# Kernel optimization log

Hardware: AMD Instinct MI355X
Metric: run time of the kernel (lower is better)

Reference implementation:

```python
import jax, jax.numpy as jnp
import numpy as np

N_HEADS = 32
HEAD_DIM = 128
TOPK = 2048
FP8_MAX = 448.0  # e4m3 max, per-token-head q quantization scale
NEG = -1e30


def _hadamard_matrix(d):
    # Sylvester construction; matches fast-hadamard-transform ordering.
    h = np.array([[1.0]], dtype=np.float32)
    while h.shape[0] < d:
        h = np.block([[h, h], [h, -h]])
    return jnp.asarray(h * d ** -0.5)  # rotate_activation scale = d^-0.5


def setup_inputs() -> dict:
    key = jax.random.key(0)
    k0, k1, k2, k3 = jax.random.split(key, 4)
    T, HID = 4096, 2048
    hidden_states = jax.random.normal(k0, (T, HID), jnp.float32)
    wq = jax.random.normal(k1, (HID, N_HEADS * HEAD_DIM), jnp.float32) * 0.02
    wk = jax.random.normal(k2, (HID, HEAD_DIM), jnp.float32) * 0.02
    ww = jax.random.normal(k3, (HID, N_HEADS), jnp.float32) * 0.02
    # Ragged causal KV bounds (compute_cu_seqlen_kv_bounds_with_cache, no cache):
    seq_lens = np.array([1024, 3072], dtype=np.int64)
    offs = np.concatenate([[0], np.cumsum(seq_lens)])
    batch_ids = np.repeat(np.arange(len(seq_lens)), seq_lens)
    ks = offs[batch_ids]                                   # start of own sequence
    local = np.arange(T) - np.repeat(offs[:-1], seq_lens)  # local query position
    ke = ks + local + 1                                    # causal end (exclusive)
    return {
        'hidden_states': hidden_states, 'wq': wq, 'wk': wk, 'ww': ww,
        'cu_seqlen_ks': jnp.asarray(ks, jnp.int32),
        'cu_seqlen_ke': jnp.asarray(ke, jnp.int32),
    }


def reference(hidden_states, wq, wk, ww, cu_seqlen_ks, cu_seqlen_ke):
    T = hidden_states.shape[0]
    Hm = _hadamard_matrix(HEAD_DIM)
    # Projections + Hadamard rotation (rotate_activation)
    q = (hidden_states @ wq).reshape(T, N_HEADS, HEAD_DIM) @ Hm   # [T,H,D]
    k = (hidden_states @ wk) @ Hm                                  # [T,D]
    # fp8-style per-(token,head) quantization of q; scale folded into weights (_scale)
    q_scale = jnp.maximum(jnp.max(jnp.abs(q), axis=-1, keepdims=True) / FP8_MAX, 1e-12)
    qq = q / q_scale                                               # [T,H,D]
    weights = hidden_states @ ww                                   # [T,H]
    softmax_scale = HEAD_DIM ** -0.5
    w_eff = weights * (N_HEADS ** -0.5) * q_scale[..., 0] * softmax_scale  # [T,H]
    # logits[t,s] = sum_h w_eff[t,h] * relu(qq[t,h] . k[s]); scan heads to avoid [T,H,S]
    def step(acc, inp):
        qh, wh = inp                                 # [T,D], [T]
        return acc + wh[:, None] * jax.nn.relu(qh @ k.T), None
    acc0 = jnp.zeros((T, T), jnp.float32)
    logits, _ = jax.lax.scan(jax.checkpoint(step), acc0,
                             (jnp.moveaxis(qq, 1, 0), w_eff.T))
    # Ragged causal window mask from cu_seqlen bounds
    s_idx = jnp.arange(T, dtype=jnp.int32)
    mask = (s_idx[None, :] >= cu_seqlen_ks[:, None]) & (s_idx[None, :] < cu_seqlen_ke[:, None])
    masked = jnp.where(mask, logits, NEG)
    vals, idx = jax.lax.top_k(masked, TOPK)
    idx = jnp.where(vals > NEG * 0.5, idx, -1)  # invalid (out-of-window) slots -> -1
    return vals, idx
```

## Files before the change

### kernel.cpp

```cpp
#include <hip/hip_runtime.h>
#include <cstdint>
#include <cstddef>

constexpr int HID = 2048;
constexpr int NH  = 32;
constexpr int HD  = 128;
constexpr int TOPK_N = 2048;
constexpr int NPAD = 4352;

typedef __attribute__((ext_vector_type(8))) short bf16x8;
typedef __attribute__((ext_vector_type(4))) float f32x4;
typedef __attribute__((ext_vector_type(8))) unsigned short u16x8;

__device__ inline unsigned short f2bf(float f) {
  unsigned u = __float_as_uint(f);
  return (unsigned short)((u + 0x7FFFu + ((u >> 16) & 1u)) >> 16);
}

__global__ __launch_bounds__(256) void convert_hs(const float* __restrict__ src,
                                                  unsigned short* __restrict__ dst) {
  size_t i = ((size_t)blockIdx.x * 256 + threadIdx.x) * 8;
  float4 v0 = *(const float4*)&src[i];
  float4 v1 = *(const float4*)&src[i + 4];
  u16x8 o;
  o[0] = f2bf(v0.x); o[1] = f2bf(v0.y); o[2] = f2bf(v0.z); o[3] = f2bf(v0.w);
  o[4] = f2bf(v1.x); o[5] = f2bf(v1.y); o[6] = f2bf(v1.z); o[7] = f2bf(v1.w);
  *(u16x8*)&dst[i] = o;
}

__global__ __launch_bounds__(256) void transpose_w(const float* __restrict__ wq,
                                                   const float* __restrict__ wk,
                                                   const float* __restrict__ ww,
                                                   unsigned short* __restrict__ WT) {
  __shared__ float tile[64][65];
  const int bx = blockIdx.x, k0 = blockIdx.y * 64;
  const int tid = threadIdx.x;
  const float* src; int stride, n0s, ncols;
  if (bx < 64)       { src = wq; stride = 4096; n0s = bx * 64;        ncols = 64; }
  else if (bx < 66)  { src = wk; stride = 128;  n0s = (bx - 64) * 64; ncols = 64; }
  else               { src = ww; stride = 32;   n0s = 0;              ncols = 32; }
  #pragma unroll
  for (int p = 0; p < 16; p++) {
    int idx = tid + p * 256;
    int r = idx >> 6, c = idx & 63;
    tile[r][c] = (c < ncols) ? src[(size_t)(k0 + r) * stride + n0s + c] : 0.f;
  }
  __syncthreads();
  const int n0 = bx * 64;
  #pragma unroll
  for (int p = 0; p < 16; p++) {
    int idx = tid + p * 256;
    int nl = idx >> 6, kc = idx & 63;
    if (nl < ncols)
      WT[(size_t)(n0 + nl) * HID + k0 + kc] = f2bf(tile[kc][nl]);
  }
}

__global__ __launch_bounds__(256) void proj_mfma(const unsigned short* __restrict__ A,
                                                 const unsigned short* __restrict__ WT,
                                                 unsigned short* __restrict__ q_pre,
                                                 unsigned short* __restrict__ k_pre,
                                                 float* __restrict__ w_pre, int T) {
  __shared__ unsigned short As[128 * 64];
  __shared__ unsigned short Bs[128 * 64];
  const int tid = threadIdx.x;
  const int lane = tid & 63, wv = tid >> 6;
  const int m0 = blockIdx.y * 128, n0 = blockIdx.x * 128;
  const int mbase = (wv & 1) * 64, nbase = (wv >> 1) * 64;
  const int s_row0 = tid >> 3, s_slot = tid & 7;
  f32x4 acc[4][4] = {};

  const unsigned short* Ag = A  + (size_t)m0 * HID + s_slot * 8;
  const unsigned short* Bg = WT + (size_t)n0 * HID + s_slot * 8;

  for (int kt = 0; kt < HID; kt += 64) {
    u16x8 av[4], bv[4];
    #pragma unroll
    for (int p = 0; p < 4; p++) {
      int row = s_row0 + p * 32;
      av[p] = *(const u16x8*)(Ag + (size_t)row * HID + kt);
      bv[p] = *(const u16x8*)(Bg + (size_t)row * HID + kt);
    }
    __syncthreads();
    #pragma unroll
    for (int p = 0; p < 4; p++) {
      int row = s_row0 + p * 32;
      int b = row * 128 + ((s_slot ^ (row & 7)) << 4);
      *(u16x8*)((char*)As + b) = av[p];
      *(u16x8*)((char*)Bs + b) = bv[p];
    }
    __syncthreads();
    #pragma unroll
    for (int kf = 0; kf < 2; kf++) {
      bf16x8 a[4], b[4];
      #pragma unroll
      for (int mi = 0; mi < 4; mi++) {
        int row = mbase + mi * 16 + (lane & 15);
        int slot = (kf * 4 + (lane >> 4)) ^ (row & 7);
        a[mi] = *(bf16x8*)((char*)As + row * 128 + slot * 16);
      }
      #pragma unroll
      for (int ni = 0; ni < 4; ni++) {
        int row = nbase + ni * 16 + (lane & 15);
        int slot = (kf * 4 + (lane >> 4)) ^ (row & 7);
        b[ni] = *(bf16x8*)((char*)Bs + row * 128 + slot * 16);
      }
      #pragma unroll
      for (int mi = 0; mi < 4; mi++)
        #pragma unroll
        for (int ni = 0; ni < 4; ni++)
          acc[mi][ni] = __builtin_amdgcn_mfma_f32_16x16x32_bf16(a[mi], b[ni], acc[mi][ni], 0, 0, 0);
    }
  }

  const int bx = blockIdx.x;
  #pragma unroll
  for (int mi = 0; mi < 4; mi++) {
    int trow = m0 + mbase + mi * 16 + ((lane >> 4) << 2);
    #pragma unroll
    for (int ni = 0; ni < 4; ni++) {
      int ncol = nbase + ni * 16 + (lane & 15);
      #pragma unroll
      for (int r = 0; r < 4; r++) {
        float v = acc[mi][ni][r];
        if (bx < 32) {
          q_pre[(size_t)(trow + r) * 4096 + bx * 128 + ncol] = f2bf(v);
        } else if (bx == 32) {
          k_pre[(size_t)(trow + r) * HD + ncol] = f2bf(v);
        } else if (ncol < NH) {
          w_pre[(size_t)(trow + r) * NH + ncol] = v * 0.015625f;
        }
      }
    }
  }
}

__global__ __launch_bounds__(256) void logits_mfma(const unsigned short* __restrict__ q,
                                                   const unsigned short* __restrict__ kp,
                                                   const float* __restrict__ w,
                                                   const int* __restrict__ ksa,
                                                   const int* __restrict__ kea,
                                                   float* __restrict__ logits, int T) {
  const int nwg = (T / 128) * (T / 128);
  const int swz = (blockIdx.x & 7) * (nwg >> 3) + (blockIdx.x >> 3);
  const int s0 = (swz & (T / 128 - 1)) * 128, t0 = (swz / (T / 128)) * 128;
  if (s0 >= kea[t0 + 127] || s0 + 128 <= ksa[t0]) return;

  __shared__ unsigned short Kt[128 * 128];
  __shared__ unsigned short Qt[128 * 128];
  __shared__ float wl[NH][128];

  const int tid = threadIdx.x;
  const int lane = tid & 63, wv = tid >> 6;
  const int mbase = (wv & 1) * 64, nbase = (wv >> 1) * 64;
  const int s_row0 = tid >> 4, s_c = tid & 15;

  #pragma unroll
  for (int p = 0; p < 8; p++) {
    int row = s_row0 + p * 16;
    u16x8 v = *(const u16x8*)(kp + (size_t)(s0 + row) * HD + s_c * 8);
    *(u16x8*)((char*)Kt + row * 256 + ((s_c ^ (row & 15)) << 4)) = v;
  }
  #pragma unroll
  for (int p = 0; p < 16; p++) {
    int idx = tid + p * 256;
    int tl = idx >> 5, h = idx & 31;
    wl[h][tl] = w[(size_t)(t0 + tl) * NH + h];
  }
  __syncthreads();

  bf16x8 bf[4][4];
  #pragma unroll
  for (int ni = 0; ni < 4; ni++)
    #pragma unroll
    for (int kf = 0; kf < 4; kf++) {
      int row = nbase + ni * 16 + (lane & 15);
      int slot = (kf * 4 + (lane >> 4)) ^ (row & 15);
      bf[ni][kf] = *(bf16x8*)((char*)Kt + row * 256 + slot * 16);
    }

  f32x4 accL[4][4] = {};
  for (int h = 0; h < NH; h++) {
    u16x8 qv[8];
    #pragma unroll
    for (int p = 0; p < 8; p++) {
      int row = s_row0 + p * 16;
      qv[p] = *(const u16x8*)(q + (size_t)(t0 + row) * (NH * HD) + h * HD + s_c * 8);
    }
    __syncthreads();
    #pragma unroll
    for (int p = 0; p < 8; p++) {
      int row = s_row0 + p * 16;
      *(u16x8*)((char*)Qt + row * 256 + ((s_c ^ (row & 15)) << 4)) = qv[p];
    }
    __syncthreads();

    #pragma unroll
    for (int mi = 0; mi < 4; mi++) {
      bf16x8 a[4];
      #pragma unroll
      for (int kf = 0; kf < 4; kf++) {
        int row = mbase + mi * 16 + (lane & 15);
        int slot = (kf * 4 + (lane >> 4)) ^ (row & 15);
        a[kf] = *(bf16x8*)((char*)Qt + row * 256 + slot * 16);
      }
      f32x4 wvv = *(f32x4*)&wl[h][mbase + mi * 16 + ((lane >> 4) << 2)];
      #pragma unroll
      for (int ni = 0; ni < 4; ni++) {
        f32x4 d = {0.f, 0.f, 0.f, 0.f};
        #pragma unroll
        for (int kf = 0; kf < 4; kf++)
          d = __builtin_amdgcn_mfma_f32_16x16x32_bf16(a[kf], bf[ni][kf], d, 0, 0, 0);
        #pragma unroll
        for (int r = 0; r < 4; r++)
          accL[mi][ni][r] += wvv[r] * fmaxf(d[r], 0.f);
      }
    }
  }

  #pragma unroll
  for (int mi = 0; mi < 4; mi++)
    #pragma unroll
    for (int ni = 0; ni < 4; ni++) {
      int trow = t0 + mbase + mi * 16 + ((lane >> 4) << 2);
      int scol = s0 + nbase + ni * 16 + (lane & 15);
      #pragma unroll
      for (int r = 0; r < 4; r++)
        logits[(size_t)(trow + r) * T + scol] = accL[mi][ni][r];
    }
}

__global__ __launch_bounds__(256) void topk_radix(const float* __restrict__ logits,
                                                  const int* __restrict__ ksa,
                                                  const int* __restrict__ kea,
                                                  float* __restrict__ vals,
                                                  float* __restrict__ idxs,
                                                  int T) {
  __shared__ unsigned keys[4096];
  __shared__ unsigned hist[256];
  __shared__ unsigned sh_bin, sh_k, out_pos, tie_taken;
  const int t = blockIdx.x;
  const int tid = threadIdx.x;
  const int ks = ksa[t];
  const int win = kea[t] - ks;
  float* vrow = vals + (size_t)t * TOPK_N;
  float* irow = idxs + (size_t)t * TOPK_N;

  const float* row = logits + (size_t)t * T + ks;
  for (int j = tid; j < win; j += 256) {
    unsigned u = __float_as_uint(row[j]);
    keys[j] = (u & 0x80000000u) ? ~u : (u | 0x80000000u);
  }
  __syncthreads();

  if (win <= TOPK_N) {
    for (int j = tid; j < TOPK_N; j += 256) {
      if (j < win) {
        unsigned m = keys[j];
        unsigned u = (m & 0x80000000u) ? (m & 0x7FFFFFFFu) : ~m;
        vrow[j] = __uint_as_float(u);
        irow[j] = (float)(ks + j);
      } else {
        vrow[j] = -1e30f;
        irow[j] = -1.0f;
      }
    }
    return;
  }

  unsigned prefix = 0, prefmask = 0;
  int k = TOPK_N;
  #pragma unroll
  for (int shift = 24; shift >= 0; shift -= 8) {
    hist[tid & 255] = 0;
    __syncthreads();
    for (int j = tid; j < win; j += 256) {
      unsigned m = keys[j];
      if ((m & prefmask) == prefix) atomicAdd(&hist[(m >> shift) & 255], 1u);
    }
    __syncthreads();
    if (tid == 0) {
      unsigned c = 0; int b = 255;
      for (; b > 0; --b) { c += hist[b]; if ((int)c >= k) break; }
      if ((int)c < k) c += hist[0];
      sh_bin = (unsigned)b;
      sh_k = (unsigned)(k - (int)(c - hist[b]));
    }
    __syncthreads();
    prefix |= sh_bin << shift;
    prefmask |= 255u << shift;
    k = (int)sh_k;
    __syncthreads();
  }
  const unsigned thr = prefix;
  const unsigned quota = (unsigned)k;

  if (tid == 0) { out_pos = 0; tie_taken = 0; }
  __syncthreads();
  for (int j = tid; j < win; j += 256) {
    unsigned m = keys[j];
    bool take = false;
    if (m > thr) take = true;
    else if (m == thr) take = (atomicAdd(&tie_taken, 1u) < quota);
    if (take) {
      unsigned p = atomicAdd(&out_pos, 1u);
      unsigned u = (m & 0x80000000u) ? (m & 0x7FFFFFFFu) : ~m;
      vrow[p] = __uint_as_float(u);
      irow[p] = (float)(ks + j);
    }
  }
}

extern "C" void kernel_launch(void* const* d_in, const int* in_sizes, int n_in,
                              void* d_out, int out_size, void* d_ws, size_t ws_size,
                              hipStream_t stream) {
  const float* hs = (const float*)d_in[0];
  const float* wq = (const float*)d_in[1];
  const float* wk = (const float*)d_in[2];
  const float* ww = (const float*)d_in[3];
  const int* ksa  = (const int*)d_in[4];
  const int* kea  = (const int*)d_in[5];
  const int T = in_sizes[0] / HID;

  char* p = (char*)d_ws;
  size_t off = 0;
  auto take = [&](size_t bytes) { char* r = p + off; off = (off + bytes + 255) & ~(size_t)255; return r; };
  unsigned short* hs_bf = (unsigned short*)take((size_t)T * HID * 2);
  unsigned short* WT    = (unsigned short*)take((size_t)NPAD * HID * 2);
  unsigned short* q_pre = (unsigned short*)take((size_t)T * NH * HD * 2);
  unsigned short* k_pre = (unsigned short*)take((size_t)T * HD * 2);
  float*          w_pre = (float*)take((size_t)T * NH * 4);
  float*          logits = (float*)take((size_t)T * T * 4);

  dim3 blk(256);
  convert_hs <<<dim3((T * HID) / 2048), blk, 0, stream>>>(hs, hs_bf);
  transpose_w<<<dim3(67, HID / 64), blk, 0, stream>>>(wq, wk, ww, WT);
  proj_mfma  <<<dim3(34, T / 128), blk, 0, stream>>>(hs_bf, WT, q_pre, k_pre, w_pre, T);
  logits_mfma<<<dim3((T / 128) * (T / 128)), blk, 0, stream>>>(q_pre, k_pre, w_pre, ksa, kea, logits, T);

  float* vals = (float*)d_out;
  float* idxs = (float*)d_out + (size_t)T * TOPK_N;
  topk_radix<<<dim3(T), blk, 0, stream>>>(logits, ksa, kea, vals, idxs, T);
}
```

Measured before the change: 432.4 us.

## Pre-pack Q/K into MFMA fragment layout and drop LDS staging in logits

Adds a repack kernel that rewrites the projected Q and K into the exact per-lane MFMA operand order. The logits kernel can then load A and B fragments straight from global memory with coalesced 16-byte loads. This removes the per-head LDS staging of Q and its two barriers per head, and the LDS K tile. The cost is an extra pass over Q and K that reads and writes about 34 MB. The fragment buffers reuse workspace that held the bf16 hidden states and transposed weights, which are no longer needed at that point.

Result: faster. 419.0 us (-3.1%).

```diff
diff --git a/kernel.cpp b/kernel.cpp
--- a/kernel.cpp
+++ b/kernel.cpp
@@ -135,75 +135,75 @@
   }
 }
 
-__global__ __launch_bounds__(256) void logits_mfma(const unsigned short* __restrict__ q,
-                                                   const unsigned short* __restrict__ kp,
+__global__ __launch_bounds__(256) void repack_frag(const unsigned short* __restrict__ src,
+                                                   unsigned short* __restrict__ dst,
+                                                   int rowstride, int log2H) {
+  __shared__ unsigned short lds[4][16][128];
+  const int tid = threadIdx.x;
+  const int u = tid >> 6, lane = tid & 63;
+  const int unit = blockIdx.x * 4 + u;
+  const int r16 = unit >> log2H, h = unit & ((1 << log2H) - 1);
+  const size_t sbase = (size_t)r16 * 16 * rowstride + h * HD;
+
+  #pragma unroll
+  for (int p = 0; p < 4; p++) {
+    int v = lane + p * 64;
+    int row = v >> 4, c8 = v & 15;
+    u16x8 x = *(const u16x8*)(src + sbase + (size_t)row * rowstride + c8 * 8);
+    *(u16x8*)&lds[u][row][((c8 ^ (row & 7)) * 8)] = x;
+  }
+  __syncthreads();
+  unsigned short* dbase = dst + ((size_t)unit * 4) * 64 * 8;
+  #pragma unroll
+  for (int kf = 0; kf < 4; kf++) {
+    int row = lane & 15, c8 = kf * 4 + (lane >> 4);
+    u16x8 x = *(u16x8*)&lds[u][row][((c8 ^ (row & 7)) * 8)];
+    *(u16x8*)(dbase + ((size_t)kf * 64 + lane) * 8) = x;
+  }
+}
+
+__global__ __launch_bounds__(256) void logits_mfma(const unsigned short* __restrict__ qf,
+                                                   const unsigned short* __restrict__ kf_,
                                                    const float* __restrict__ w,
                                                    const int* __restrict__ ksa,
                                                    const int* __restrict__ kea,
                                                    float* __restrict__ logits, int T) {
-  const int nwg = (T / 128) * (T / 128);
+  const int nt = T / 128;
+  const int nwg = nt * nt;
   const int swz = (blockIdx.x & 7) * (nwg >> 3) + (blockIdx.x >> 3);
-  const int s0 = (swz & (T / 128 - 1)) * 128, t0 = (swz / (T / 128)) * 128;
+  const int s0 = (swz & (nt - 1)) * 128, t0 = (swz / nt) * 128;
   if (s0 >= kea[t0 + 127] || s0 + 128 <= ksa[t0]) return;
 
-  __shared__ unsigned short Kt[128 * 128];
-  __shared__ unsigned short Qt[128 * 128];
   __shared__ float wl[NH][128];
-
   const int tid = threadIdx.x;
   const int lane = tid & 63, wv = tid >> 6;
   const int mbase = (wv & 1) * 64, nbase = (wv >> 1) * 64;
-  const int s_row0 = tid >> 4, s_c = tid & 15;
-
-  #pragma unroll
-  for (int p = 0; p < 8; p++) {
-    int row = s_row0 + p * 16;
-    u16x8 v = *(const u16x8*)(kp + (size_t)(s0 + row) * HD + s_c * 8);
-    *(u16x8*)((char*)Kt + row * 256 + ((s_c ^ (row & 15)) << 4)) = v;
-  }
+
   #pragma unroll
   for (int p = 0; p < 16; p++) {
     int idx = tid + p * 256;
     int tl = idx >> 5, h = idx & 31;
     wl[h][tl] = w[(size_t)(t0 + tl) * NH + h];
   }
-  __syncthreads();
 
   bf16x8 bf[4][4];
+  const int sbase16 = (s0 + nbase) >> 4;
   #pragma unroll
   for (int ni = 0; ni < 4; ni++)
     #pragma unroll
-    for (int kf = 0; kf < 4; kf++) {
-      int row = nbase + ni * 16 + (lane & 15);
-      int slot = (kf * 4 + (lane >> 4)) ^ (row & 15);
-      bf[ni][kf] = *(bf16x8*)((char*)Kt + row * 256 + slot * 16);
-    }
+    for (int kf = 0; kf < 4; kf++)
+      bf[ni][kf] = *(const bf16x8*)(kf_ + (((size_t)(sbase16 + ni) * 4 + kf) * 64 + lane) * 8);
+  __syncthreads();
 
   f32x4 accL[4][4] = {};
+  const int tbase16 = (t0 + mbase) >> 4;
   for (int h = 0; h < NH; h++) {
-    u16x8 qv[8];
-    #pragma unroll
-    for (int p = 0; p < 8; p++) {
-      int row = s_row0 + p * 16;
-      qv[p] = *(const u16x8*)(q + (size_t)(t0 + row) * (NH * HD) + h * HD + s_c * 8);
-    }
-    __syncthreads();
-    #pragma unroll
-    for (int p = 0; p < 8; p++) {
-      int row = s_row0 + p * 16;
-      *(u16x8*)((char*)Qt + row * 256 + ((s_c ^ (row & 15)) << 4)) = qv[p];
-    }
-    __syncthreads();
-
     #pragma unroll
     for (int mi = 0; mi < 4; mi++) {
       bf16x8 a[4];
       #pragma unroll
-      for (int kf = 0; kf < 4; kf++) {
-        int row = mbase + mi * 16 + (lane & 15);
-        int slot = (kf * 4 + (lane >> 4)) ^ (row & 15);
-        a[kf] = *(bf16x8*)((char*)Qt + row * 256 + slot * 16);
-      }
+      for (int kf = 0; kf < 4; kf++)
+        a[kf] = *(const bf16x8*)(qf + ((((size_t)(tbase16 + mi) * NH + h) * 4 + kf) * 64 + lane) * 8);
       f32x4 wvv = *(f32x4*)&wl[h][mbase + mi * 16 + ((lane >> 4) << 2)];
       #pragma unroll
       for (int ni = 0; ni < 4; ni++) {
@@ -332,11 +332,16 @@
   float*          w_pre = (float*)take((size_t)T * NH * 4);
   float*          logits = (float*)take((size_t)T * T * 4);
 
+  unsigned short* q_frag = (unsigned short*)d_ws;
+  unsigned short* k_frag = q_frag + (size_t)(T / 16) * NH * 4 * 64 * 8;
+
   dim3 blk(256);
   convert_hs <<<dim3((T * HID) / 2048), blk, 0, stream>>>(hs, hs_bf);
   transpose_w<<<dim3(67, HID / 64), blk, 0, stream>>>(wq, wk, ww, WT);
   proj_mfma  <<<dim3(34, T / 128), blk, 0, stream>>>(hs_bf, WT, q_pre, k_pre, w_pre, T);
-  logits_mfma<<<dim3((T / 128) * (T / 128)), blk, 0, stream>>>(q_pre, k_pre, w_pre, ksa, kea, logits, T);
+  repack_frag<<<dim3((T / 16) * NH / 4), blk, 0, stream>>>(q_pre, q_frag, NH * HD, 5);
+  repack_frag<<<dim3((T / 16) / 4), blk, 0, stream>>>(k_pre, k_frag, HD, 0);
+  logits_mfma<<<dim3((T / 128) * (T / 128)), blk, 0, stream>>>(q_frag, k_frag, w_pre, ksa, kea, logits, T);
 
   float* vals = (float*)d_out;
   float* idxs = (float*)d_out + (size_t)T * TOPK_N;
```
